# Kernel optimization log

Measured on AMD Instinct MI355X. Metric: run time of the kernel, lower is better.

## Reference

```python
import jax, jax.numpy as jnp
import numpy as np
from jax import lax


def _gauss1d(size, sigma):
    k = np.arange(size, dtype=np.float32) - (size - 1) / 2.0
    k = np.exp(-0.5 * (k / sigma) ** 2)
    return k / k.sum()


def _make_kernel(scale, sigma):
    # make_odd
    kx, ky, kz = [s + 1 if s % 2 == 0 else s for s in scale]
    kH = _gauss1d(kx, sigma)
    kW = _gauss1d(ky, sigma)
    kD = _gauss1d(kz, sigma)
    kern = kH[:, None, None] * kW[None, :, None] * kD[None, None, :]  # (kx, ky, kz)
    kern = np.transpose(kern, (2, 0, 1))  # permute(2,0,1) -> (kz, kx, ky)
    return jnp.asarray(kern, dtype=jnp.float32)


def setup_inputs() -> dict:
    key = jax.random.key(0)
    x = jax.random.normal(key, (2, 1, 256, 256, 256), dtype=jnp.float32)
    kernel0 = _make_kernel((2, 2, 2), 1.0)  # (3,3,3)
    kernel1 = _make_kernel((4, 4, 4), 1.0)  # (5,5,5)
    return {"x": x, "kernel0": kernel0, "kernel1": kernel1}


def _blur_down(x, kernel, stride):
    # replicate pad by k//2 per spatial dim, then depthwise (C=1) conv3d.
    pad = [(0, 0), (0, 0)] + [(k // 2, k // 2) for k in kernel.shape]
    xp = jnp.pad(x, pad, mode='edge')
    # strided VALID conv == full blur followed by [::s] slicing (output ceil(H/s))
    return lax.conv_general_dilated(
        xp, kernel[None, None].astype(x.dtype),
        window_strides=stride, padding='VALID',
        dimension_numbers=('NCDHW', 'OIDHW', 'NCDHW'))


def reference(x, kernel0, kernel1):
    d1 = _blur_down(x, kernel0, (2, 2, 2))  # (2,1,128,128,128)
    d2 = _blur_down(x, kernel1, (4, 4, 4))  # (2,1,64,64,64)
    return (x, d1, d2)
```

## Files before the change

### kernel.cpp

```cpp
#include <hip/hip_runtime.h>

#define S_IN 256
#define IN_PER_BATCH (S_IN * S_IN * S_IN)
#define D1_PER_BATCH (128 * 128 * 128)
#define D2_PER_BATCH (64 * 64 * 64)
#define X_ELEMS (2 * IN_PER_BATCH)
#define D1_ELEMS (2 * D1_PER_BATCH)
#define D2_ELEMS (2 * D2_PER_BATCH)

#define LXR 40
#define NROW 144
#define BUFV 1536
#define BUFF (BUFV * 4)
#define NBLK 16384

__device__ __forceinline__ void gload_lds16(const float* g, float* l) {
    __builtin_amdgcn_global_load_lds(
        (const __attribute__((address_space(1))) void*)g,
        (__attribute__((address_space(3))) void*)l, 16, 0, 0);
}

__global__ __launch_bounds__(256, 6) void fused_pyramid(
    const float* __restrict__ x, const float* __restrict__ k0,
    const float* __restrict__ k1, float* __restrict__ out0,
    float* __restrict__ out1, float* __restrict__ out2)
{
    __shared__ float ls[BUFF];
    __shared__ float kw0[9][4];
    __shared__ float kw1[25][8];

    const int tid = threadIdx.x;
    if (tid < 27) kw0[tid / 3][tid % 3] = k0[tid];
    else if (tid >= 32 && tid < 157) {
        int t = tid - 32;
        kw1[t / 5][t % 5] = k1[t];
    }

    const int bx  = blockIdx.x;
    const int lin = (bx & 7) * 2048 + (bx >> 3);
    const int wt = lin & 7;
    const int hy = (lin >> 3) & 31;
    const int dz = (lin >> 8) & 31;
    const int n  = lin >> 13;

    const int x0 = wt << 5;
    const int y0 = hy << 3;
    const int z0 = dz << 3;
    const bool edge = (wt == 0);

    const float* xb = x + (size_t)n * IN_PER_BATCH;

    {
        float* lb = ls + (tid << 2);
#pragma unroll
        for (int i = 0; i < 6; ++i) {
            int v = tid + (i << 8);
            int row = v / 10;
            int j = v - row * 10;
            int lz = row / 12;
            int ly = row - lz * 12;
            int gz = z0 + lz - 2; gz = gz < 0 ? 0 : (gz > 255 ? 255 : gz);
            int gy = y0 + ly - 2; gy = gy < 0 ? 0 : (gy > 255 ? 255 : gy);
            int gx = x0 - 4 + (j << 2); gx = gx < 0 ? 0 : (gx > 252 ? 252 : gx);
            gload_lds16(xb + (((size_t)gz << 16) + (gy << 8) + gx),
                        lb + (size_t)i * 1024);
        }
    }

    float pv = 0.0f;
    int plz = 0, ply = 0;
    const bool pact = edge && (tid < NROW);
    if (pact) {
        plz = tid / 12;
        ply = tid - plz * 12;
        int gz = z0 + plz - 2; gz = gz < 0 ? 0 : (gz > 255 ? 255 : gz);
        int gy = y0 + ply - 2; gy = gy < 0 ? 0 : (gy > 255 ? 255 : gy);
        pv = xb[((size_t)gz << 16) + (gy << 8)];
    }

    __syncthreads();
    if (edge) {
        if (pact)
            *reinterpret_cast<float2*>(
                &ls[(plz * 12 + ply) * LXR + 2]) = make_float2(pv, pv);
        __syncthreads();
    }

    {
        float* ob0 = out0 + (size_t)n * IN_PER_BATCH
                   + (((size_t)dz << 3) << 16) + (y0 << 8) + x0;
#pragma unroll
        for (int k = 0; k < 2; ++k) {
            int v = tid + (k << 8);
            int jj = v & 7;
            int rowc = v >> 3;
            int lzc = rowc >> 3, lyc = rowc & 7;
            float4 val = *reinterpret_cast<const float4*>(
                &ls[((lzc + 2) * 12 + (lyc + 2)) * LXR + 4 + (jj << 2)]);
            *reinterpret_cast<float4*>(
                &ob0[((size_t)lzc << 16) + (lyc << 8) + (jj << 2)]) = val;
        }
    }

    {
        const int ox = tid & 15, oy = (tid >> 4) & 3, oz = tid >> 6;
        const float* base = ls + ((2 * oz + 1) * 12 + (2 * oy + 1)) * LXR + 2 * ox + 2;
        float acc = 0.0f;
#pragma unroll
        for (int a = 0; a < 3; ++a)
#pragma unroll
            for (int b = 0; b < 3; ++b) {
                const float* lr = base + (a * 12 + b) * LXR;
                float2 v0 = *reinterpret_cast<const float2*>(lr);
                float2 v1 = *reinterpret_cast<const float2*>(lr + 2);
                float4 kr = *reinterpret_cast<const float4*>(&kw0[a * 3 + b][0]);
                acc = fmaf(kr.x, v0.y, acc);
                acc = fmaf(kr.y, v1.x, acc);
                acc = fmaf(kr.z, v1.y, acc);
            }
        float* ob1 = out1 + (size_t)n * D1_PER_BATCH
                   + (((size_t)dz << 2) << 14) + ((hy << 2) << 7) + (wt << 4);
        ob1[(oz << 14) + (oy << 7) + ox] = acc;
    }

    {
        const int q = tid & 7;
        const int o = tid >> 3;
        const int ox = o & 7, oy = (o >> 3) & 1, oz = o >> 4;
        float acc = 0.0f;
#pragma unroll
        for (int m = 0; m < 4; ++m) {
            int r = q + (m << 3);
            if (r < 25) {
                int a = r / 5, b = r - 5 * a;
                const float* lr = ls + ((4 * oz + a) * 12 + (4 * oy + b)) * LXR + 4 * ox;
                float4 A4 = *reinterpret_cast<const float4*>(lr);
                float4 B4 = *reinterpret_cast<const float4*>(lr + 4);
                float4 kr = *reinterpret_cast<const float4*>(&kw1[r][0]);
                float k4 = kw1[r][4];
                acc = fmaf(kr.x, A4.z, acc);
                acc = fmaf(kr.y, A4.w, acc);
                acc = fmaf(kr.z, B4.x, acc);
                acc = fmaf(kr.w, B4.y, acc);
                acc = fmaf(k4,   B4.z, acc);
            }
        }
        acc += __shfl_xor(acc, 1);
        acc += __shfl_xor(acc, 2);
        acc += __shfl_xor(acc, 4);
        if (q == 0) {
            float* ob2 = out2 + (size_t)n * D2_PER_BATCH
                       + (((size_t)dz << 1) << 12) + ((hy << 1) << 6) + (wt << 3);
            ob2[(oz << 12) + (oy << 6) + ox] = acc;
        }
    }
}

extern "C" void kernel_launch(void* const* d_in, const int* in_sizes, int n_in,
                              void* d_out, int out_size, void* d_ws, size_t ws_size,
                              hipStream_t stream) {
    const float* x  = (const float*)d_in[0];
    const float* k0 = (const float*)d_in[1];
    const float* k1 = (const float*)d_in[2];

    float* out0 = (float*)d_out;
    float* out1 = out0 + X_ELEMS;
    float* out2 = out1 + D1_ELEMS;

    fused_pyramid<<<NBLK, 256, 0, stream>>>(x, k0, k1, out0, out1, out2);
}
```

Measured before the change: 294.4 us.

## Copy passthrough directly from global, split blur work across thread halves

The identity output is now loaded straight from global memory into registers and stored before the barrier, instead of being read back from LDS afterwards. The two blur computations are split across thread halves so they run concurrently. The first half computes two adjacent d1 outputs per thread with float4 LDS reads and reads the 3x3x3 weights directly from global memory instead of staging them in LDS. The second half computes d2 with four lanes per output instead of eight. This shortens the post-barrier critical path and cuts LDS traffic, at the cost of re-reading x for the passthrough (mostly cache hits) and heavier per-thread work.

```diff
diff --git a/kernel.cpp b/kernel.cpp
--- a/kernel.cpp
+++ b/kernel.cpp
@@ -26,15 +26,9 @@
     float* __restrict__ out1, float* __restrict__ out2)
 {
     __shared__ float ls[BUFF];
-    __shared__ float kw0[9][4];
     __shared__ float kw1[25][8];
 
     const int tid = threadIdx.x;
-    if (tid < 27) kw0[tid / 3][tid % 3] = k0[tid];
-    else if (tid >= 32 && tid < 157) {
-        int t = tid - 32;
-        kw1[t / 5][t % 5] = k1[t];
-    }
 
     const int bx  = blockIdx.x;
     const int lin = (bx & 7) * 2048 + (bx >> 3);
@@ -49,6 +43,30 @@
     const bool edge = (wt == 0);
 
     const float* xb = x + (size_t)n * IN_PER_BATCH;
+
+    float4 pt0, pt1;
+    {
+        const float* gsrc = xb + (((size_t)z0) << 16) + (y0 << 8) + x0;
+        int v0 = tid,        jj0 = v0 & 7, rc0 = v0 >> 3;
+        int v1 = tid + 256,  jj1 = v1 & 7, rc1 = v1 >> 3;
+        pt0 = *reinterpret_cast<const float4*>(
+            gsrc + (((size_t)(rc0 >> 3)) << 16) + ((rc0 & 7) << 8) + (jj0 << 2));
+        pt1 = *reinterpret_cast<const float4*>(
+            gsrc + (((size_t)(rc1 >> 3)) << 16) + ((rc1 & 7) << 8) + (jj1 << 2));
+    }
+
+    float pv = 0.0f;
+    int plz = 0, ply = 0;
+    const bool pact = edge && (tid < NROW);
+    if (pact) {
+        plz = tid / 12;
+        ply = tid - plz * 12;
+        int gz = z0 + plz - 2; gz = gz < 0 ? 0 : (gz > 255 ? 255 : gz);
+        int gy = y0 + ply - 2; gy = gy < 0 ? 0 : (gy > 255 ? 255 : gy);
+        pv = xb[((size_t)gz << 16) + (gy << 8)];
+    }
+
+    if (tid < 125) kw1[tid / 5][tid % 5] = k1[tid];
 
     {
         float* lb = ls + (tid << 2);
@@ -67,15 +85,15 @@
         }
     }
 
-    float pv = 0.0f;
-    int plz = 0, ply = 0;
-    const bool pact = edge && (tid < NROW);
-    if (pact) {
-        plz = tid / 12;
-        ply = tid - plz * 12;
-        int gz = z0 + plz - 2; gz = gz < 0 ? 0 : (gz > 255 ? 255 : gz);
-        int gy = y0 + ply - 2; gy = gy < 0 ? 0 : (gy > 255 ? 255 : gy);
-        pv = xb[((size_t)gz << 16) + (gy << 8)];
+    {
+        float* ob0 = out0 + (size_t)n * IN_PER_BATCH
+                   + (((size_t)z0) << 16) + (y0 << 8) + x0;
+        int v0 = tid,        jj0 = v0 & 7, rc0 = v0 >> 3;
+        int v1 = tid + 256,  jj1 = v1 & 7, rc1 = v1 >> 3;
+        *reinterpret_cast<float4*>(
+            &ob0[(((size_t)(rc0 >> 3)) << 16) + ((rc0 & 7) << 8) + (jj0 << 2)]) = pt0;
+        *reinterpret_cast<float4*>(
+            &ob0[(((size_t)(rc1 >> 3)) << 16) + ((rc1 & 7) << 8) + (jj1 << 2)]) = pt1;
     }
 
     __syncthreads();
@@ -86,54 +104,45 @@
         __syncthreads();
     }
 
-    {
-        float* ob0 = out0 + (size_t)n * IN_PER_BATCH
-                   + (((size_t)dz << 3) << 16) + (y0 << 8) + x0;
-#pragma unroll
-        for (int k = 0; k < 2; ++k) {
-            int v = tid + (k << 8);
-            int jj = v & 7;
-            int rowc = v >> 3;
-            int lzc = rowc >> 3, lyc = rowc & 7;
-            float4 val = *reinterpret_cast<const float4*>(
-                &ls[((lzc + 2) * 12 + (lyc + 2)) * LXR + 4 + (jj << 2)]);
-            *reinterpret_cast<float4*>(
-                &ob0[((size_t)lzc << 16) + (lyc << 8) + (jj << 2)]) = val;
-        }
-    }
-
-    {
-        const int ox = tid & 15, oy = (tid >> 4) & 3, oz = tid >> 6;
-        const float* base = ls + ((2 * oz + 1) * 12 + (2 * oy + 1)) * LXR + 2 * ox + 2;
-        float acc = 0.0f;
+    if (tid < 128) {
+        const int p  = tid & 7;
+        const int oy = (tid >> 3) & 3;
+        const int oz = tid >> 5;
+        const float* base = ls + ((2 * oz + 1) * 12 + (2 * oy + 1)) * LXR + (p << 2);
+        float acc0 = 0.0f, acc1 = 0.0f;
 #pragma unroll
         for (int a = 0; a < 3; ++a)
 #pragma unroll
             for (int b = 0; b < 3; ++b) {
                 const float* lr = base + (a * 12 + b) * LXR;
-                float2 v0 = *reinterpret_cast<const float2*>(lr);
-                float2 v1 = *reinterpret_cast<const float2*>(lr + 2);
-                float4 kr = *reinterpret_cast<const float4*>(&kw0[a * 3 + b][0]);
-                acc = fmaf(kr.x, v0.y, acc);
-                acc = fmaf(kr.y, v1.x, acc);
-                acc = fmaf(kr.z, v1.y, acc);
+                float4 A  = *reinterpret_cast<const float4*>(lr);
+                float4 Bv = *reinterpret_cast<const float4*>(lr + 4);
+                float kA = k0[(a * 3 + b) * 3 + 0];
+                float kB = k0[(a * 3 + b) * 3 + 1];
+                float kC = k0[(a * 3 + b) * 3 + 2];
+                acc0 = fmaf(kA, A.w,  acc0);
+                acc0 = fmaf(kB, Bv.x, acc0);
+                acc0 = fmaf(kC, Bv.y, acc0);
+                acc1 = fmaf(kA, Bv.y, acc1);
+                acc1 = fmaf(kB, Bv.z, acc1);
+                acc1 = fmaf(kC, Bv.w, acc1);
             }
         float* ob1 = out1 + (size_t)n * D1_PER_BATCH
                    + (((size_t)dz << 2) << 14) + ((hy << 2) << 7) + (wt << 4);
-        ob1[(oz << 14) + (oy << 7) + ox] = acc;
-    }
-
-    {
-        const int q = tid & 7;
-        const int o = tid >> 3;
+        *reinterpret_cast<float2*>(
+            &ob1[(oz << 14) + (oy << 7) + (p << 1)]) = make_float2(acc0, acc1);
+    } else {
+        const int t = tid - 128;
+        const int q = t & 3;
+        const int o = t >> 2;
         const int ox = o & 7, oy = (o >> 3) & 1, oz = o >> 4;
         float acc = 0.0f;
 #pragma unroll
-        for (int m = 0; m < 4; ++m) {
-            int r = q + (m << 3);
+        for (int m = 0; m < 7; ++m) {
+            int r = q + (m << 2);
             if (r < 25) {
                 int a = r / 5, b = r - 5 * a;
-                const float* lr = ls + ((4 * oz + a) * 12 + (4 * oy + b)) * LXR + 4 * ox;
+                const float* lr = ls + ((4 * oz + a) * 12 + (4 * oy + b)) * LXR + (ox << 2);
                 float4 A4 = *reinterpret_cast<const float4*>(lr);
                 float4 B4 = *reinterpret_cast<const float4*>(lr + 4);
                 float4 kr = *reinterpret_cast<const float4*>(&kw1[r][0]);
@@ -147,7 +156,6 @@
         }
         acc += __shfl_xor(acc, 1);
         acc += __shfl_xor(acc, 2);
-        acc += __shfl_xor(acc, 4);
         if (q == 0) {
             float* ob2 = out2 + (size_t)n * D2_PER_BATCH
                        + (((size_t)dz << 1) << 12) + ((hy << 1) << 6) + (wt << 3);
```

Result: slower. 303.1 us (+3.0%).
